# Optimization experiments

Hardware: AMD Instinct MI355X
Metric: run time of the kernel (lower is better)

## Reference

```python
import jax, jax.numpy as jnp
import numpy as np

N, K, D = 64, 512, 256
LEAKY_SLOPE = 0.01  # torch LeakyReLU default


def setup_inputs() -> dict:
    key = jax.random.key(0)
    k_x, k_w, k_b, k_aw, k_ab = jax.random.split(key, 5)
    x = jax.random.normal(k_x, (N, K, D), dtype=jnp.float32)
    # nn.Linear(D, D): weight [D, D], bias [D]
    W_w = jax.random.normal(k_w, (D, D), dtype=jnp.float32) / np.sqrt(D)
    W_b = jax.random.normal(k_b, (D,), dtype=jnp.float32) * 0.01
    # nn.Linear(2D, 1): weight [2D] (squeezed), bias scalar
    att_w = jax.random.normal(k_aw, (2 * D,), dtype=jnp.float32) / np.sqrt(2 * D)
    att_b = jax.random.normal(k_ab, (), dtype=jnp.float32) * 0.01
    return {"x": x, "W_w": W_w, "W_b": W_b, "att_w": att_w, "att_b": att_b}


def reference(x, W_w, W_b, att_w, att_b):
    n, k, d = x.shape
    # h = W(x): [N,K,D]
    h = jnp.einsum('nkd,ed->nke', x, W_w) + W_b
    # attention score e[n,i,j] = leaky_relu(concat(h_i, h_j) @ att_w + b)
    # split att_w to avoid materializing the [N,K,K,2D] concat tensor
    s_src = h @ att_w[:d]   # [N,K] contribution of h_i (first half of concat)
    s_dst = h @ att_w[d:]   # [N,K] contribution of h_j (second half)
    e = jax.nn.leaky_relu(s_src[:, :, None] + s_dst[:, None, :] + att_b,
                          negative_slope=LEAKY_SLOPE)  # [N,K,K]
    a = jax.nn.softmax(e, axis=2)
    # faithful to original einsum 'nkj,nkd->nkd' (sums attention over j,
    # then scales h elementwise)
    out = jnp.einsum('nkj,nkd->nkd', a, h)
    return jax.nn.relu(out)
```

## Files before the change

### kernel.cpp

```cpp
#include <hip/hip_runtime.h>
#include <hip/hip_bf16.h>


#define DD 256
#define M_TOTAL 32768
#define LWS 264

typedef short bf16x8 __attribute__((ext_vector_type(8)));
typedef float floatx16 __attribute__((ext_vector_type(16)));

#define BAR() asm volatile("s_waitcnt lgkmcnt(0)\n\ts_barrier" ::: "memory")

__device__ inline bf16x8 pack8(float4 p0, float4 p1) {
    __hip_bfloat162 q0 = __float22bfloat162_rn(make_float2(p0.x, p0.y));
    __hip_bfloat162 q1 = __float22bfloat162_rn(make_float2(p0.z, p0.w));
    __hip_bfloat162 q2 = __float22bfloat162_rn(make_float2(p1.x, p1.y));
    __hip_bfloat162 q3 = __float22bfloat162_rn(make_float2(p1.z, p1.w));
    union { bf16x8 v; unsigned u[4]; } r;
    union { __hip_bfloat162 h; unsigned u; } c;
    c.h = q0; r.u[0] = c.u;
    c.h = q1; r.u[1] = c.u;
    c.h = q2; r.u[2] = c.u;
    c.h = q3; r.u[3] = c.u;
    return r.v;
}

__device__ inline void load_tile(const float* __restrict__ x, int m0,
                                 int r0, int c0, float4 P[4]) {
    const float* s0 = x + (m0 + r0) * DD + c0;
    const float* s1 = x + (m0 + 16 + r0) * DD + c0;
    P[0] = *(const float4*)(s0);
    P[1] = *(const float4*)(s0 + 4);
    P[2] = *(const float4*)(s1);
    P[3] = *(const float4*)(s1 + 4);
}

__device__ inline void write_lx(unsigned short* lx, int r0, int c0,
                                const float4 P[4]) {
    *(bf16x8*)(lx + r0 * LWS + c0)        = pack8(P[0], P[1]);
    *(bf16x8*)(lx + (16 + r0) * LWS + c0) = pack8(P[2], P[3]);
}

__device__ inline void compute_tile(const unsigned short* ap,
                                    const unsigned short* bp, floatx16& acc) {
#pragma unroll
    for (int i = 0; i < 16; ++i) acc[i] = 0.f;
#pragma unroll
    for (int s = 0; s < 16; ++s) {
        bf16x8 af = *(const bf16x8*)(ap + s * 16);
        bf16x8 bf = *(const bf16x8*)(bp + s * 16);
        acc = __builtin_amdgcn_mfma_f32_32x32x16_bf16(af, bf, acc, 0, 0, 0);
    }
}

__device__ inline void store_tile(float* ob, int m0, int lh, float bias,
                                  const floatx16& acc) {
#pragma unroll
    for (int r = 0; r < 16; ++r) {
        const int m = m0 + (r & 3) + 8 * (r >> 2) + 4 * lh;
        float v = acc[r] + bias;
        v = v > 0.f ? v : 0.f;
        __builtin_nontemporal_store(v, ob + m * DD);
    }
}

__global__ void __launch_bounds__(512, 1)
fcgat_gemm(const float* __restrict__ x, const float* __restrict__ W,
           const float* __restrict__ Wbias, float* __restrict__ out) {
    __shared__ __align__(16) unsigned short lw[256 * LWS];
    __shared__ __align__(16) unsigned short lx[32 * LWS];

    const int tid   = threadIdx.x;
    const int r0    = tid >> 5;
    const int c0    = (tid & 31) * 8;
    const int mbase = blockIdx.x * 128;

    float4 Pa[4], Pb[4];
    load_tile(x, mbase + 0,  r0, c0, Pa);
    load_tile(x, mbase + 32, r0, c0, Pb);

#pragma unroll
    for (int k = 0; k < 16; ++k) {
        const int r = r0 + 16 * k;
        const float* ws = W + r * DD + c0;
        float4 a0 = *(const float4*)(ws);
        float4 a1 = *(const float4*)(ws + 4);
        *(bf16x8*)(lw + r * LWS + c0) = pack8(a0, a1);
    }

    write_lx(lx, r0, c0, Pa);
    BAR();

    const int lane = tid & 63;
    const int wave = tid >> 6;
    const int ln   = lane & 31;
    const int lh   = lane >> 5;

    const unsigned short* ap = lx + ln * LWS + lh * 8;
    const unsigned short* bp = lw + (wave * 32 + ln) * LWS + lh * 8;
    const float bias = Wbias[wave * 32 + ln];
    float* ob = out + wave * 32 + ln;

    floatx16 acc;

    compute_tile(ap, bp, acc);
    BAR();
    write_lx(lx, r0, c0, Pb);
    load_tile(x, mbase + 64, r0, c0, Pa);
    BAR();
    store_tile(ob, mbase + 0, lh, bias, acc);

    compute_tile(ap, bp, acc);
    BAR();
    write_lx(lx, r0, c0, Pa);
    load_tile(x, mbase + 96, r0, c0, Pb);
    BAR();
    store_tile(ob, mbase + 32, lh, bias, acc);

    compute_tile(ap, bp, acc);
    BAR();
    write_lx(lx, r0, c0, Pb);
    BAR();
    store_tile(ob, mbase + 64, lh, bias, acc);

    compute_tile(ap, bp, acc);
    store_tile(ob, mbase + 96, lh, bias, acc);
}

extern "C" void kernel_launch(void* const* d_in, const int* in_sizes, int n_in,
                              void* d_out, int out_size, void* d_ws, size_t ws_size,
                              hipStream_t stream) {
    const float* x    = (const float*)d_in[0];
    const float* W_w  = (const float*)d_in[1];
    const float* W_b  = (const float*)d_in[2];
    float* out = (float*)d_out;

    fcgat_gemm<<<M_TOTAL / 128, 512, 0, stream>>>(x, W_w, W_b, out);
}
```

Baseline: 90.23 us.

## Pre-cast W to bf16 MFMA fragments and keep B operands in registers

A small pre-kernel converts W to bf16 once, laid out in the exact per-lane MFMA fragment order, and stores it in the workspace. The main kernel then loads each wave's B fragments straight into registers, so W no longer goes through LDS. LDS use drops to two small x tiles, which are double-buffered so one of the two barriers per tile can be removed. The cost is an extra kernel launch and 64 more registers per lane for the held fragments.

```diff
diff --git a/kernel.cpp b/kernel.cpp
--- a/kernel.cpp
+++ b/kernel.cpp
@@ -25,6 +25,20 @@
     return r.v;
 }
 
+__global__ void cast_w_frag(const float* __restrict__ W,
+                            unsigned short* __restrict__ Wb) {
+    const int gid  = blockIdx.x * 256 + threadIdx.x;
+    const int w    = gid >> 10;
+    const int s    = (gid >> 6) & 15;
+    const int lane = gid & 63;
+    const int e    = w * 32 + (lane & 31);
+    const int k0   = s * 16 + (lane >> 5) * 8;
+    const float* src = W + e * DD + k0;
+    float4 a0 = *(const float4*)(src);
+    float4 a1 = *(const float4*)(src + 4);
+    *(bf16x8*)(Wb + gid * 8) = pack8(a0, a1);
+}
+
 __device__ inline void load_tile(const float* __restrict__ x, int m0,
                                  int r0, int c0, float4 P[4]) {
     const float* s0 = x + (m0 + r0) * DD + c0;
@@ -42,14 +56,13 @@
 }
 
 __device__ inline void compute_tile(const unsigned short* ap,
-                                    const unsigned short* bp, floatx16& acc) {
+                                    const bf16x8 Bf[16], floatx16& acc) {
 #pragma unroll
     for (int i = 0; i < 16; ++i) acc[i] = 0.f;
 #pragma unroll
     for (int s = 0; s < 16; ++s) {
         bf16x8 af = *(const bf16x8*)(ap + s * 16);
-        bf16x8 bf = *(const bf16x8*)(bp + s * 16);
-        acc = __builtin_amdgcn_mfma_f32_32x32x16_bf16(af, bf, acc, 0, 0, 0);
+        acc = __builtin_amdgcn_mfma_f32_32x32x16_bf16(af, Bf[s], acc, 0, 0, 0);
     }
 }
 
@@ -65,65 +78,60 @@
 }
 
 __global__ void __launch_bounds__(512, 1)
-fcgat_gemm(const float* __restrict__ x, const float* __restrict__ W,
+fcgat_gemm(const float* __restrict__ x, const unsigned short* __restrict__ Wb,
            const float* __restrict__ Wbias, float* __restrict__ out) {
-    __shared__ __align__(16) unsigned short lw[256 * LWS];
-    __shared__ __align__(16) unsigned short lx[32 * LWS];
+    __shared__ __align__(16) unsigned short lx0[32 * LWS];
+    __shared__ __align__(16) unsigned short lx1[32 * LWS];
 
     const int tid   = threadIdx.x;
     const int r0    = tid >> 5;
     const int c0    = (tid & 31) * 8;
     const int mbase = blockIdx.x * 128;
+    const int lane  = tid & 63;
+    const int wave  = tid >> 6;
 
     float4 Pa[4], Pb[4];
     load_tile(x, mbase + 0,  r0, c0, Pa);
     load_tile(x, mbase + 32, r0, c0, Pb);
 
+    bf16x8 Bf[16];
+    {
+        const unsigned short* wb = Wb + wave * 8192 + lane * 8;
 #pragma unroll
-    for (int k = 0; k < 16; ++k) {
-        const int r = r0 + 16 * k;
-        const float* ws = W + r * DD + c0;
-        float4 a0 = *(const float4*)(ws);
-        float4 a1 = *(const float4*)(ws + 4);
-        *(bf16x8*)(lw + r * LWS + c0) = pack8(a0, a1);
+        for (int s = 0; s < 16; ++s)
+            Bf[s] = *(const bf16x8*)(wb + s * 512);
     }
 
-    write_lx(lx, r0, c0, Pa);
+    write_lx(lx0, r0, c0, Pa);
     BAR();
 
-    const int lane = tid & 63;
-    const int wave = tid >> 6;
-    const int ln   = lane & 31;
-    const int lh   = lane >> 5;
-
-    const unsigned short* ap = lx + ln * LWS + lh * 8;
-    const unsigned short* bp = lw + (wave * 32 + ln) * LWS + lh * 8;
+    const int ln = lane & 31;
+    const int lh = lane >> 5;
+    const unsigned short* ap0 = lx0 + ln * LWS + lh * 8;
+    const unsigned short* ap1 = lx1 + ln * LWS + lh * 8;
     const float bias = Wbias[wave * 32 + ln];
     float* ob = out + wave * 32 + ln;
 
     floatx16 acc;
 
-    compute_tile(ap, bp, acc);
-    BAR();
-    write_lx(lx, r0, c0, Pb);
+    compute_tile(ap0, Bf, acc);
+    write_lx(lx1, r0, c0, Pb);
     load_tile(x, mbase + 64, r0, c0, Pa);
     BAR();
     store_tile(ob, mbase + 0, lh, bias, acc);
 
-    compute_tile(ap, bp, acc);
-    BAR();
-    write_lx(lx, r0, c0, Pa);
+    compute_tile(ap1, Bf, acc);
+    write_lx(lx0, r0, c0, Pa);
     load_tile(x, mbase + 96, r0, c0, Pb);
     BAR();
     store_tile(ob, mbase + 32, lh, bias, acc);
 
-    compute_tile(ap, bp, acc);
-    BAR();
-    write_lx(lx, r0, c0, Pb);
+    compute_tile(ap0, Bf, acc);
+    write_lx(lx1, r0, c0, Pb);
     BAR();
     store_tile(ob, mbase + 64, lh, bias, acc);
 
-    compute_tile(ap, bp, acc);
+    compute_tile(ap1, Bf, acc);
     store_tile(ob, mbase + 96, lh, bias, acc);
 }
 
@@ -134,6 +142,8 @@
     const float* W_w  = (const float*)d_in[1];
     const float* W_b  = (const float*)d_in[2];
     float* out = (float*)d_out;
+    unsigned short* Wb = (unsigned short*)d_ws;
 
-    fcgat_gemm<<<M_TOTAL / 128, 512, 0, stream>>>(x, W_w, W_b, out);
+    cast_w_frag<<<32, 256, 0, stream>>>(W_w, Wb);
+    fcgat_gemm<<<M_TOTAL / 128, 512, 0, stream>>>(x, Wb, W_b, out);
 }
```

After: 90.27 us. About the same (+0.0%).
